# Performance work log

Hardware: AMD Instinct MI355X
Metric: run time of the kernel (lower is better)

The kernel has to match this reference:

```python
import jax, jax.numpy as jnp
import numpy as np

B, N, D, H = 8, 1024, 768, 12
HD = D // H


def setup_inputs() -> dict:
    key = jax.random.key(0)
    ks = jax.random.split(key, 13)
    s = 0.02
    return {
        "q": jax.random.normal(ks[0], (B, N, D), jnp.float32),
        "k": jax.random.normal(ks[1], (B, N, D), jnp.float32),
        "v": jax.random.normal(ks[2], (B, N, D), jnp.float32),
        "attn_bias": jax.random.normal(ks[3], (B, H, N, N), jnp.float32),
        "attn_mask": jnp.ones((B, N, N), jnp.int32),
        "Wq": jax.random.normal(ks[4], (D, D), jnp.float32) * s,
        "bq": jnp.zeros((D,), jnp.float32),
        "Wk": jax.random.normal(ks[5], (D, D), jnp.float32) * s,
        "bk": jnp.zeros((D,), jnp.float32),
        "Wv": jax.random.normal(ks[6], (D, D), jnp.float32) * s,
        "bv": jnp.zeros((D,), jnp.float32),
        "Wo": jax.random.normal(ks[7], (D, D), jnp.float32) * s,
        "bo": jnp.zeros((D,), jnp.float32),
    }


def reference(q, k, v, attn_bias, attn_mask, Wq, bq, Wk, bk, Wv, bv, Wo, bo):
    scale = jnp.sqrt(jnp.float32(HD))
    # projections; nn.Linear computes x @ W.T + b
    qh = (q @ Wq.T + bq).reshape(B, N, H, HD).transpose(0, 2, 1, 3)  # [B,H,N,hd]
    kh = (k @ Wk.T + bk).reshape(B, N, H, HD).transpose(0, 2, 1, 3)
    vh = (v @ Wv.T + bv).reshape(B, N, H, HD).transpose(0, 2, 1, 3)
    attn = jnp.einsum("bhqd,bhkd->bhqk", qh, kh) / scale
    attn = attn + attn_bias  # Graphormer edge/spatial bias
    attn = jnp.where(attn_mask[:, None, :, :] == 0, -jnp.inf, attn)
    attn = jax.nn.softmax(attn, axis=-1)
    out = jnp.einsum("bhqk,bhkd->bhqd", attn, vh)  # [B,H,N,hd]
    out = out.transpose(0, 2, 1, 3).reshape(B, N, D)
    return out @ Wo.T + bo
```

## Files before the change

kernel.cpp:

```cpp
#include <hip/hip_runtime.h>
#include <hip/hip_bf16.h>

using f32x4  = __attribute__((ext_vector_type(4))) float;
using i32x4  = __attribute__((ext_vector_type(4))) int;
using bf16x8 = __attribute__((ext_vector_type(8))) short;
using bf16x4 = __attribute__((ext_vector_type(4))) short;

constexpr int BATCH = 8, SEQ = 1024, DIM = 768, NHEAD = 12, HDIM = 64;
constexpr int MROWS = BATCH * SEQ;

__device__ __forceinline__ short f2bf(float f) {
    union { float f; unsigned u; } x; x.f = f;
    unsigned r = (x.u + 0x7fffu + ((x.u >> 16) & 1u)) >> 16;
    return (short)r;
}
__device__ __forceinline__ float fexp2(float x) { return __builtin_amdgcn_exp2f(x); }

__device__ __forceinline__ bf16x8 cvt8(const float* p) {
    const f32x4 x0 = *(const f32x4*)p;
    const f32x4 x1 = *(const f32x4*)(p + 4);
    bf16x8 r;
    #pragma unroll
    for (int j = 0; j < 4; ++j) { r[j] = f2bf(x0[j]); r[4 + j] = f2bf(x1[j]); }
    return r;
}

__global__ __launch_bounds__(256)
void cvt3(const float* __restrict__ a, const float* __restrict__ b,
          const float* __restrict__ c, short* __restrict__ oa,
          short* __restrict__ ob, short* __restrict__ oc, int n8) {
    const int stride = gridDim.x * 256;
    for (int i = blockIdx.x * 256 + threadIdx.x; i < n8; i += stride) {
        const long base = (long)i * 8;
        *(bf16x8*)(oa + base) = cvt8(a + base);
        *(bf16x8*)(ob + base) = cvt8(b + base);
        *(bf16x8*)(oc + base) = cvt8(c + base);
    }
}

__global__ __launch_bounds__(256)
void cvt4(const float* __restrict__ a, const float* __restrict__ b,
          const float* __restrict__ c, const float* __restrict__ d,
          short* __restrict__ oa, short* __restrict__ ob,
          short* __restrict__ oc, short* __restrict__ od, int n8) {
    const int stride = gridDim.x * 256;
    for (int i = blockIdx.x * 256 + threadIdx.x; i < n8; i += stride) {
        const long base = (long)i * 8;
        *(bf16x8*)(oa + base) = cvt8(a + base);
        *(bf16x8*)(ob + base) = cvt8(b + base);
        *(bf16x8*)(oc + base) = cvt8(c + base);
        *(bf16x8*)(od + base) = cvt8(d + base);
    }
}

template <int OMODE>
__global__ __launch_bounds__(256, 4)
void gemm_bf16(const short* __restrict__ A, const short* __restrict__ W,
               const float* __restrict__ bias, void* __restrict__ Cout, float oscale) {
    constexpr int K  = DIM;
    constexpr int NT = DIM / 128;
    __shared__ short As[128][72];
    __shared__ short Bs[128][72];

    const int bm = blockIdx.x / NT, bn = blockIdx.x % NT;
    const int m0 = bm * 128, n0 = bn * 128;
    const int t = threadIdx.x;
    const int lane = t & 63, w = t >> 6;
    const int wm = (w >> 1) * 64, wn = (w & 1) * 64;
    const int l16 = lane & 15, lg = lane >> 4;

    const int sr = t >> 1, sc = (t & 1) * 16;
    const short* aptr = A + (long)(m0 + sr) * K + sc;
    const short* wptr = W + (long)(n0 + sr) * K + sc;

    bf16x8 ra0 = *(const bf16x8*)(aptr);
    bf16x8 ra1 = *(const bf16x8*)(aptr + 8);
    bf16x8 rw0 = *(const bf16x8*)(wptr);
    bf16x8 rw1 = *(const bf16x8*)(wptr + 8);

    f32x4 acc[4][4] = {};

    for (int k0 = 0; k0 < K; k0 += 32) {
        *(bf16x8*)&As[sr][sc]     = ra0;
        *(bf16x8*)&As[sr][sc + 8] = ra1;
        *(bf16x8*)&Bs[sr][sc]     = rw0;
        *(bf16x8*)&Bs[sr][sc + 8] = rw1;
        if (k0 + 32 < K) {
            ra0 = *(const bf16x8*)(aptr + k0 + 32);
            ra1 = *(const bf16x8*)(aptr + k0 + 40);
            rw0 = *(const bf16x8*)(wptr + k0 + 32);
            rw1 = *(const bf16x8*)(wptr + k0 + 40);
        }
        __syncthreads();

        bf16x8 af[4], bfg[4];
        const int kc = lg * 8;
        #pragma unroll
        for (int mi = 0; mi < 4; ++mi)
            af[mi] = *(const bf16x8*)&As[wm + mi * 16 + l16][kc];
        #pragma unroll
        for (int ni = 0; ni < 4; ++ni)
            bfg[ni] = *(const bf16x8*)&Bs[wn + ni * 16 + l16][kc];
        #pragma unroll
        for (int mi = 0; mi < 4; ++mi)
            #pragma unroll
            for (int ni = 0; ni < 4; ++ni)
                acc[mi][ni] = __builtin_amdgcn_mfma_f32_16x16x32_bf16(
                    af[mi], bfg[ni], acc[mi][ni], 0, 0, 0);
        __syncthreads();
    }

    #pragma unroll
    for (int mi = 0; mi < 4; ++mi) {
        const int row = m0 + wm + mi * 16 + lg * 4;
        #pragma unroll
        for (int ni = 0; ni < 4; ++ni) {
            const int col = n0 + wn + ni * 16 + l16;
            const float bv = bias[col];
            #pragma unroll
            for (int j = 0; j < 4; ++j) {
                float val = (acc[mi][ni][j] + bv) * oscale;
                if constexpr (OMODE == 0) {
                    ((short*)Cout)[(long)(row + j) * DIM + col] = f2bf(val);
                } else if constexpr (OMODE == 1) {
                    ((float*)Cout)[(long)(row + j) * DIM + col] = val;
                } else {
                    const int bb = row / SEQ;
                    const int tok = (row % SEQ) + j;
                    const int hh = col >> 6, dd = col & 63;
                    const long base = ((long)(bb * NHEAD + hh) * 16 + (tok >> 6)) * 4096;
                    if constexpr (OMODE == 2)
                        ((short*)Cout)[base + dd * 64 + (tok & 63)] = f2bf(val);
                    else
                        ((short*)Cout)[base + (tok & 63) * 64 + dd] = f2bf(val);
                }
            }
        }
    }
}

__global__ __launch_bounds__(256, 4)
void attn_kernel(const short* __restrict__ Qp, const short* __restrict__ Kt,
                 const short* __restrict__ Vt, const float* __restrict__ bias,
                 const int* __restrict__ mask, short* __restrict__ Op) {
    __shared__ float Bsm[64][68];
    __shared__ short Ks[64][72];
    __shared__ short Vs[64][72];

    const int d = blockIdx.x;
    const int lgc = (d & 7) * 192 + (d >> 3);
    const int qt = lgc & 15, pair = lgc >> 4;
    const int h = pair % NHEAD, b = pair / NHEAD;

    const int t = threadIdx.x, lane = t & 63, w = t >> 6;
    const int l16 = lane & 15, lg = lane >> 4;
    const int ql = w * 16 + l16;

    const int qrow = qt * 64 + ql;
    const short* qptr = Qp + (long)(b * SEQ + qrow) * DIM + h * HDIM + lg * 8;
    const bf16x8 qf0 = *(const bf16x8*)qptr;
    const bf16x8 qf1 = *(const bf16x8*)(qptr + 32);

    const short* ktile = Kt + (long)pair * 16 * 4096;
    const short* vtile = Vt + (long)pair * 16 * 4096;

    const int srow = t >> 4, scol = (t & 15) * 4;
    const float* bst = bias + ((long)pair * SEQ + qt * 64 + srow) * SEQ + scol;
    const int*   mst = mask + ((long)b * SEQ + qt * 64 + srow) * SEQ + scol;

    const int kr = t >> 3, kc = (t & 7) * 8;

    short* prow = (short*)&Bsm[ql][0];

    f32x4 acc_o[4] = {};
    float m_run = -1e30f, l_run = 0.f;
    constexpr float L2E = 1.4426950408889634f;

    f32x4 br[4]; i32x4 mr[4];
    bf16x8 kst0, kst1, vst0, vst1;

    auto issue_bm = [&](int kt) {
        #pragma unroll
        for (int i = 0; i < 4; ++i) {
            br[i] = *(const f32x4*)(bst + (long)i * 16 * SEQ + kt * 64);
            mr[i] = *(const i32x4*)(mst + (long)i * 16 * SEQ + kt * 64);
        }
    };
    auto issue_kv = [&](int kt) {
        const short* kp = ktile + kt * 4096 + t * 8;
        const short* vp = vtile + kt * 4096 + t * 8;
        kst0 = *(const bf16x8*)kp;
        kst1 = *(const bf16x8*)(kp + 2048);
        vst0 = *(const bf16x8*)vp;
        vst1 = *(const bf16x8*)(vp + 2048);
    };
    auto write_bm = [&]() {
        #pragma unroll
        for (int i = 0; i < 4; ++i) {
            f32x4 o;
            #pragma unroll
            for (int j = 0; j < 4; ++j) o[j] = mr[i][j] ? br[i][j] : -1e30f;
            *(f32x4*)&Bsm[i * 16 + srow][scol] = o;
        }
    };
    auto write_kv = [&]() {
        *(bf16x8*)&Ks[kr][kc]      = kst0;
        *(bf16x8*)&Ks[kr + 32][kc] = kst1;
        *(bf16x8*)&Vs[kr][kc]      = vst0;
        *(bf16x8*)&Vs[kr + 32][kc] = vst1;
    };

    auto compute = [&]() {
        f32x4 s[4];
        #pragma unroll
        for (int c = 0; c < 4; ++c) {
            const bf16x8 kb0 = *(const bf16x8*)&Ks[c * 16 + l16][lg * 8];
            const bf16x8 kb1 = *(const bf16x8*)&Ks[c * 16 + l16][32 + lg * 8];
            f32x4 ci = *(const f32x4*)&Bsm[ql][c * 16 + lg * 4];
            ci   = __builtin_amdgcn_mfma_f32_16x16x32_bf16(kb0, qf0, ci, 0, 0, 0);
            s[c] = __builtin_amdgcn_mfma_f32_16x16x32_bf16(kb1, qf1, ci, 0, 0, 0);
        }
        bf16x8 vb0[4], vb1[4];
        #pragma unroll
        for (int df = 0; df < 4; ++df) {
            vb0[df] = *(const bf16x8*)&Vs[df * 16 + l16][lg * 8];
            vb1[df] = *(const bf16x8*)&Vs[df * 16 + l16][32 + lg * 8];
        }

        float mt = -1e30f;
        #pragma unroll
        for (int c = 0; c < 4; ++c)
            #pragma unroll
            for (int j = 0; j < 4; ++j)
                mt = fmaxf(mt, s[c][j]);
        mt = fmaxf(mt, __shfl_xor(mt, 16));
        mt = fmaxf(mt, __shfl_xor(mt, 32));
        const float mn = fmaxf(m_run, mt);
        const float alpha = fexp2((m_run - mn) * L2E);
        m_run = mn;
        const float nm = -mn * L2E;

        float lt = 0.f;
        #pragma unroll
        for (int c = 0; c < 4; ++c) {
            bf16x4 pk;
            #pragma unroll
            for (int j = 0; j < 4; ++j) {
                const float e = fexp2(fmaf(s[c][j], L2E, nm));
                lt += e;
                pk[j] = f2bf(e);
            }
            *(bf16x4*)(prow + c * 16 + lg * 4) = pk;
        }
        lt += __shfl_xor(lt, 16);
        lt += __shfl_xor(lt, 32);
        l_run = l_run * alpha + lt;

        float al[4];
        #pragma unroll
        for (int j = 0; j < 4; ++j) al[j] = __shfl(alpha, lg * 4 + j);
        #pragma unroll
        for (int df = 0; df < 4; ++df)
            #pragma unroll
            for (int j = 0; j < 4; ++j)
                acc_o[df][j] *= al[j];

        const bf16x8 pa0 = *(const bf16x8*)(prow + lg * 8);
        const bf16x8 pa1 = *(const bf16x8*)(prow + 32 + lg * 8);
        #pragma unroll
        for (int df = 0; df < 4; ++df) {
            acc_o[df] = __builtin_amdgcn_mfma_f32_16x16x32_bf16(pa0, vb0[df], acc_o[df], 0, 0, 0);
            acc_o[df] = __builtin_amdgcn_mfma_f32_16x16x32_bf16(pa1, vb1[df], acc_o[df], 0, 0, 0);
        }
    };

    issue_bm(0);
    issue_kv(0);
    write_bm();
    write_kv();
    __syncthreads();

    for (int kt = 0; kt < 16; ++kt) {
        if (kt < 15) { issue_bm(kt + 1); issue_kv(kt + 1); }
        compute();
        if (kt < 15) {
            __syncthreads();
            write_bm();
            write_kv();
            __syncthreads();
        }
    }

    float linv[4];
    #pragma unroll
    for (int j = 0; j < 4; ++j)
        linv[j] = 1.f / fmaxf(__shfl(l_run, lg * 4 + j), 1e-20f);

    #pragma unroll
    for (int df = 0; df < 4; ++df) {
        #pragma unroll
        for (int j = 0; j < 4; ++j) {
            const float val = acc_o[df][j] * linv[j];
            const int row = b * SEQ + qt * 64 + w * 16 + lg * 4 + j;
            const int col = h * HDIM + df * 16 + l16;
            Op[(long)row * DIM + col] = f2bf(val);
        }
    }
}

extern "C" void kernel_launch(void* const* d_in, const int* in_sizes, int n_in,
                              void* d_out, int out_size, void* d_ws, size_t ws_size,
                              hipStream_t stream) {
    const float* q         = (const float*)d_in[0];
    const float* k         = (const float*)d_in[1];
    const float* v         = (const float*)d_in[2];
    const float* attn_bias = (const float*)d_in[3];
    const int*   attn_mask = (const int*)d_in[4];
    const float* Wq = (const float*)d_in[5];
    const float* bq = (const float*)d_in[6];
    const float* Wk = (const float*)d_in[7];
    const float* bk = (const float*)d_in[8];
    const float* Wv = (const float*)d_in[9];
    const float* bv = (const float*)d_in[10];
    const float* Wo = (const float*)d_in[11];
    const float* bo = (const float*)d_in[12];
    float* out = (float*)d_out;

    const long NED = (long)MROWS * DIM;
    const long WED = (long)DIM * DIM;
    short* Qp  = (short*)d_ws;
    short* Kp  = Qp + NED;
    short* Vp  = Kp + NED;
    short* Op  = Vp + NED;
    short* qb  = Op + NED;
    short* kb  = qb + NED;
    short* vb  = kb + NED;
    short* Wqb = vb + NED;
    short* Wkb = Wqb + WED;
    short* Wvb = Wkb + WED;
    short* Wob = Wvb + WED;

    const dim3 blk(256);

    cvt3<<<2048, blk, 0, stream>>>(q, k, v, qb, kb, vb, (int)(NED / 8));
    cvt4<<<288, blk, 0, stream>>>(Wq, Wk, Wv, Wo, Wqb, Wkb, Wvb, Wob, (int)(WED / 8));

    const int gemm_grid = (MROWS / 128) * (DIM / 128);
    gemm_bf16<0><<<gemm_grid, blk, 0, stream>>>(qb, Wqb, bq, Qp, 0.125f);
    gemm_bf16<3><<<gemm_grid, blk, 0, stream>>>(kb, Wkb, bk, Kp, 1.0f);
    gemm_bf16<2><<<gemm_grid, blk, 0, stream>>>(vb, Wvb, bv, Vp, 1.0f);

    const int attn_grid = BATCH * NHEAD * (SEQ / 64);
    attn_kernel<<<attn_grid, blk, 0, stream>>>(Qp, Kp, Vp, attn_bias, attn_mask, Op);

    gemm_bf16<1><<<gemm_grid, blk, 0, stream>>>(Op, Wob, bo, out, 1.0f);
}
```

Measured before the change: 280.2 us.

## Store K/V in MFMA fragment order and load directly from global in attention

The QKV projection epilogue now writes K and V in a fragment-major layout, so each attention lane can load its MFMA operand with one contiguous 16-byte global read. This lets the attention kernel drop the K/V shared-memory staging and its LDS writes and reads. The three projection GEMMs are merged into one launch, the bias stream uses nontemporal loads, and MFMA sections get raised wave priority. The cost is that K/V operands are now read from global/L2 inside the compute loop without prefetch, so load latency is exposed to the math.

After: 273.8 us. 2.3% less time.

```diff
diff --git a/kernel.cpp b/kernel.cpp
--- a/kernel.cpp
+++ b/kernel.cpp
@@ -23,6 +23,15 @@
     #pragma unroll
     for (int j = 0; j < 4; ++j) { r[j] = f2bf(x0[j]); r[4 + j] = f2bf(x1[j]); }
     return r;
+}
+
+__device__ __forceinline__ long kfrag_addr(int tok, int dd) {
+    return ((long)(tok >> 6)) * 4096 + ((tok & 63) >> 4) * 1024 + (dd >> 5) * 512
+         + ((dd >> 3) & 3) * 128 + (tok & 15) * 8 + (dd & 7);
+}
+__device__ __forceinline__ long vfrag_addr(int tok, int dd) {
+    return ((long)(tok >> 6)) * 4096 + (dd >> 4) * 1024 + ((tok >> 5) & 1) * 512
+         + ((tok >> 3) & 3) * 128 + (dd & 15) * 8 + (tok & 7);
 }
 
 __global__ __launch_bounds__(256)
@@ -53,16 +62,26 @@
     }
 }
 
-template <int OMODE>
 __global__ __launch_bounds__(256, 4)
-void gemm_bf16(const short* __restrict__ A, const short* __restrict__ W,
-               const float* __restrict__ bias, void* __restrict__ Cout, float oscale) {
+void gemm_qkv(const short* __restrict__ qb, const short* __restrict__ kb,
+              const short* __restrict__ vbp,
+              const short* __restrict__ Wqb, const short* __restrict__ Wkb,
+              const short* __restrict__ Wvb,
+              const float* __restrict__ bq, const float* __restrict__ bk,
+              const float* __restrict__ bv,
+              short* __restrict__ Qp, short* __restrict__ Kp, short* __restrict__ Vp) {
     constexpr int K  = DIM;
     constexpr int NT = DIM / 128;
     __shared__ short As[128][72];
     __shared__ short Bs[128][72];
 
-    const int bm = blockIdx.x / NT, bn = blockIdx.x % NT;
+    const int sub = blockIdx.x % 3;
+    const int bid = blockIdx.x / 3;
+    const short* A = sub == 0 ? qb : sub == 1 ? kb : vbp;
+    const short* W = sub == 0 ? Wqb : sub == 1 ? Wkb : Wvb;
+    const float* bias = sub == 0 ? bq : sub == 1 ? bk : bv;
+
+    const int bm = bid / NT, bn = bid % NT;
     const int m0 = bm * 128, n0 = bn * 128;
     const int t = threadIdx.x;
     const int lane = t & 63, w = t >> 6;
@@ -113,28 +132,96 @@
     #pragma unroll
     for (int mi = 0; mi < 4; ++mi) {
         const int row = m0 + wm + mi * 16 + lg * 4;
+        const int bb = row / SEQ;
         #pragma unroll
         for (int ni = 0; ni < 4; ++ni) {
             const int col = n0 + wn + ni * 16 + l16;
             const float bv = bias[col];
+            const int hh = col >> 6, dd = col & 63;
             #pragma unroll
             for (int j = 0; j < 4; ++j) {
-                float val = (acc[mi][ni][j] + bv) * oscale;
-                if constexpr (OMODE == 0) {
-                    ((short*)Cout)[(long)(row + j) * DIM + col] = f2bf(val);
-                } else if constexpr (OMODE == 1) {
-                    ((float*)Cout)[(long)(row + j) * DIM + col] = val;
+                float val = acc[mi][ni][j] + bv;
+                if (sub == 0) {
+                    Qp[(long)(row + j) * DIM + col] = f2bf(val * 0.125f);
                 } else {
-                    const int bb = row / SEQ;
                     const int tok = (row % SEQ) + j;
-                    const int hh = col >> 6, dd = col & 63;
-                    const long base = ((long)(bb * NHEAD + hh) * 16 + (tok >> 6)) * 4096;
-                    if constexpr (OMODE == 2)
-                        ((short*)Cout)[base + dd * 64 + (tok & 63)] = f2bf(val);
+                    const long pbase = (long)(bb * NHEAD + hh) * 65536;
+                    if (sub == 1)
+                        Kp[pbase + kfrag_addr(tok, dd)] = f2bf(val);
                     else
-                        ((short*)Cout)[base + (tok & 63) * 64 + dd] = f2bf(val);
+                        Vp[pbase + vfrag_addr(tok, dd)] = f2bf(val);
                 }
             }
+        }
+    }
+}
+
+__global__ __launch_bounds__(256, 4)
+void gemm_out(const short* __restrict__ A, const short* __restrict__ W,
+              const float* __restrict__ bias, float* __restrict__ Cout) {
+    constexpr int K  = DIM;
+    constexpr int NT = DIM / 128;
+    __shared__ short As[128][72];
+    __shared__ short Bs[128][72];
+
+    const int bm = blockIdx.x / NT, bn = blockIdx.x % NT;
+    const int m0 = bm * 128, n0 = bn * 128;
+    const int t = threadIdx.x;
+    const int lane = t & 63, w = t >> 6;
+    const int wm = (w >> 1) * 64, wn = (w & 1) * 64;
+    const int l16 = lane & 15, lg = lane >> 4;
+
+    const int sr = t >> 1, sc = (t & 1) * 16;
+    const short* aptr = A + (long)(m0 + sr) * K + sc;
+    const short* wptr = W + (long)(n0 + sr) * K + sc;
+
+    bf16x8 ra0 = *(const bf16x8*)(aptr);
+    bf16x8 ra1 = *(const bf16x8*)(aptr + 8);
+    bf16x8 rw0 = *(const bf16x8*)(wptr);
+    bf16x8 rw1 = *(const bf16x8*)(wptr + 8);
+
+    f32x4 acc[4][4] = {};
+
+    for (int k0 = 0; k0 < K; k0 += 32) {
+        *(bf16x8*)&As[sr][sc]     = ra0;
+        *(bf16x8*)&As[sr][sc + 8] = ra1;
+        *(bf16x8*)&Bs[sr][sc]     = rw0;
+        *(bf16x8*)&Bs[sr][sc + 8] = rw1;
+        if (k0 + 32 < K) {
+            ra0 = *(const bf16x8*)(aptr + k0 + 32);
+            ra1 = *(const bf16x8*)(aptr + k0 + 40);
+            rw0 = *(const bf16x8*)(wptr + k0 + 32);
+            rw1 = *(const bf16x8*)(wptr + k0 + 40);
+        }
+        __syncthreads();
+
+        bf16x8 af[4], bfg[4];
+        const int kc = lg * 8;
+        #pragma unroll
+        for (int mi = 0; mi < 4; ++mi)
+            af[mi] = *(const bf16x8*)&As[wm + mi * 16 + l16][kc];
+        #pragma unroll
+        for (int ni = 0; ni < 4; ++ni)
+            bfg[ni] = *(const bf16x8*)&Bs[wn + ni * 16 + l16][kc];
+        #pragma unroll
+        for (int mi = 0; mi < 4; ++mi)
+            #pragma unroll
+            for (int ni = 0; ni < 4; ++ni)
+                acc[mi][ni] = __builtin_amdgcn_mfma_f32_16x16x32_bf16(
+                    af[mi], bfg[ni], acc[mi][ni], 0, 0, 0);
+        __syncthreads();
+    }
+
+    #pragma unroll
+    for (int mi = 0; mi < 4; ++mi) {
+        const int row = m0 + wm + mi * 16 + lg * 4;
+        #pragma unroll
+        for (int ni = 0; ni < 4; ++ni) {
+            const int col = n0 + wn + ni * 16 + l16;
+            const float bv = bias[col];
+            #pragma unroll
+            for (int j = 0; j < 4; ++j)
+                Cout[(long)(row + j) * DIM + col] = acc[mi][ni][j] + bv;
         }
     }
 }
@@ -144,8 +231,6 @@
                  const short* __restrict__ Vt, const float* __restrict__ bias,
                  const int* __restrict__ mask, short* __restrict__ Op) {
     __shared__ float Bsm[64][68];
-    __shared__ short Ks[64][72];
-    __shared__ short Vs[64][72];
 
     const int d = blockIdx.x;
     const int lgc = (d & 7) * 192 + (d >> 3);
@@ -161,15 +246,13 @@
     const bf16x8 qf0 = *(const bf16x8*)qptr;
     const bf16x8 qf1 = *(const bf16x8*)(qptr + 32);
 
-    const short* ktile = Kt + (long)pair * 16 * 4096;
-    const short* vtile = Vt + (long)pair * 16 * 4096;
+    const short* ktile = Kt + (long)pair * 65536 + lane * 8;
+    const short* vtile = Vt + (long)pair * 65536 + lane * 8;
 
     const int srow = t >> 4, scol = (t & 15) * 4;
     const float* bst = bias + ((long)pair * SEQ + qt * 64 + srow) * SEQ + scol;
     const int*   mst = mask + ((long)b * SEQ + qt * 64 + srow) * SEQ + scol;
 
-    const int kr = t >> 3, kc = (t & 7) * 8;
-
     short* prow = (short*)&Bsm[ql][0];
 
     f32x4 acc_o[4] = {};
@@ -177,22 +260,13 @@
     constexpr float L2E = 1.4426950408889634f;
 
     f32x4 br[4]; i32x4 mr[4];
-    bf16x8 kst0, kst1, vst0, vst1;
 
     auto issue_bm = [&](int kt) {
         #pragma unroll
         for (int i = 0; i < 4; ++i) {
-            br[i] = *(const f32x4*)(bst + (long)i * 16 * SEQ + kt * 64);
+            br[i] = __builtin_nontemporal_load((const f32x4*)(bst + (long)i * 16 * SEQ + kt * 64));
             mr[i] = *(const i32x4*)(mst + (long)i * 16 * SEQ + kt * 64);
         }
-    };
-    auto issue_kv = [&](int kt) {
-        const short* kp = ktile + kt * 4096 + t * 8;
-        const short* vp = vtile + kt * 4096 + t * 8;
-        kst0 = *(const bf16x8*)kp;
-        kst1 = *(const bf16x8*)(kp + 2048);
-        vst0 = *(const bf16x8*)vp;
-        vst1 = *(const bf16x8*)(vp + 2048);
     };
     auto write_bm = [&]() {
         #pragma unroll
@@ -203,29 +277,25 @@
             *(f32x4*)&Bsm[i * 16 + srow][scol] = o;
         }
     };
-    auto write_kv = [&]() {
-        *(bf16x8*)&Ks[kr][kc]      = kst0;
-        *(bf16x8*)&Ks[kr + 32][kc] = kst1;
-        *(bf16x8*)&Vs[kr][kc]      = vst0;
-        *(bf16x8*)&Vs[kr + 32][kc] = vst1;
-    };
-
-    auto compute = [&]() {
+
+    auto compute = [&](int kt) {
+        const short* kf = ktile + kt * 4096;
+        const short* vf = vtile + kt * 4096;
+
         f32x4 s[4];
+        __builtin_amdgcn_s_setprio(1);
         #pragma unroll
         for (int c = 0; c < 4; ++c) {
-            const bf16x8 kb0 = *(const bf16x8*)&Ks[c * 16 + l16][lg * 8];
-            const bf16x8 kb1 = *(const bf16x8*)&Ks[c * 16 + l16][32 + lg * 8];
+            const bf16x8 kb = *(const bf16x8*)(kf + c * 1024);
             f32x4 ci = *(const f32x4*)&Bsm[ql][c * 16 + lg * 4];
-            ci   = __builtin_amdgcn_mfma_f32_16x16x32_bf16(kb0, qf0, ci, 0, 0, 0);
-            s[c] = __builtin_amdgcn_mfma_f32_16x16x32_bf16(kb1, qf1, ci, 0, 0, 0);
-        }
-        bf16x8 vb0[4], vb1[4];
-        #pragma unroll
-        for (int df = 0; df < 4; ++df) {
-            vb0[df] = *(const bf16x8*)&Vs[df * 16 + l16][lg * 8];
-            vb1[df] = *(const bf16x8*)&Vs[df * 16 + l16][32 + lg * 8];
-        }
+            s[c] = __builtin_amdgcn_mfma_f32_16x16x32_bf16(kb, qf0, ci, 0, 0, 0);
+        }
+        #pragma unroll
+        for (int c = 0; c < 4; ++c) {
+            const bf16x8 kb = *(const bf16x8*)(kf + c * 1024 + 512);
+            s[c] = __builtin_amdgcn_mfma_f32_16x16x32_bf16(kb, qf1, s[c], 0, 0, 0);
+        }
+        __builtin_amdgcn_s_setprio(0);
 
         float mt = -1e30f;
         #pragma unroll
@@ -267,26 +337,30 @@
 
         const bf16x8 pa0 = *(const bf16x8*)(prow + lg * 8);
         const bf16x8 pa1 = *(const bf16x8*)(prow + 32 + lg * 8);
+        __builtin_amdgcn_s_setprio(1);
         #pragma unroll
         for (int df = 0; df < 4; ++df) {
-            acc_o[df] = __builtin_amdgcn_mfma_f32_16x16x32_bf16(pa0, vb0[df], acc_o[df], 0, 0, 0);
-            acc_o[df] = __builtin_amdgcn_mfma_f32_16x16x32_bf16(pa1, vb1[df], acc_o[df], 0, 0, 0);
-        }
+            const bf16x8 vb = *(const bf16x8*)(vf + df * 1024);
+            acc_o[df] = __builtin_amdgcn_mfma_f32_16x16x32_bf16(pa0, vb, acc_o[df], 0, 0, 0);
+        }
+        #pragma unroll
+        for (int df = 0; df < 4; ++df) {
+            const bf16x8 vb = *(const bf16x8*)(vf + df * 1024 + 512);
+            acc_o[df] = __builtin_amdgcn_mfma_f32_16x16x32_bf16(pa1, vb, acc_o[df], 0, 0, 0);
+        }
+        __builtin_amdgcn_s_setprio(0);
     };
 
     issue_bm(0);
-    issue_kv(0);
     write_bm();
-    write_kv();
     __syncthreads();
 
     for (int kt = 0; kt < 16; ++kt) {
-        if (kt < 15) { issue_bm(kt + 1); issue_kv(kt + 1); }
-        compute();
+        if (kt < 15) issue_bm(kt + 1);
+        compute(kt);
         if (kt < 15) {
             __syncthreads();
             write_bm();
-            write_kv();
             __syncthreads();
         }
     }
@@ -346,12 +420,11 @@
     cvt4<<<288, blk, 0, stream>>>(Wq, Wk, Wv, Wo, Wqb, Wkb, Wvb, Wob, (int)(WED / 8));
 
     const int gemm_grid = (MROWS / 128) * (DIM / 128);
-    gemm_bf16<0><<<gemm_grid, blk, 0, stream>>>(qb, Wqb, bq, Qp, 0.125f);
-    gemm_bf16<3><<<gemm_grid, blk, 0, stream>>>(kb, Wkb, bk, Kp, 1.0f);
-    gemm_bf16<2><<<gemm_grid, blk, 0, stream>>>(vb, Wvb, bv, Vp, 1.0f);
+    gemm_qkv<<<3 * gemm_grid, blk, 0, stream>>>(qb, kb, vb, Wqb, Wkb, Wvb,
+                                                bq, bk, bv, Qp, Kp, Vp);
 
     const int attn_grid = BATCH * NHEAD * (SEQ / 64);
     attn_kernel<<<attn_grid, blk, 0, stream>>>(Qp, Kp, Vp, attn_bias, attn_mask, Op);
 
-    gemm_bf16<1><<<gemm_grid, blk, 0, stream>>>(Op, Wob, bo, out, 1.0f);
-}
+    gemm_out<<<gemm_grid, blk, 0, stream>>>(Op, Wob, bo, out);
+}
```
